# Kernel optimization log

Measured on AMD Instinct MI355X. Metric: run time of the kernel, lower is better.

Reference implementation:

```python
import jax, jax.numpy as jnp
import numpy as np

NUM_USERS = 100000
NUM_ITEMS = 50000
EMB_DIM = 64
NUM_LAYERS = 3
NUM_EDGES = 1000000


def _xavier(key, shape):
    fan_in, fan_out = shape[-1], shape[-2] if len(shape) > 1 else shape[-1]
    limit = float(np.sqrt(6.0 / (fan_in + fan_out)))
    return jax.random.uniform(key, shape, jnp.float32, -limit, limit)


def setup_inputs() -> dict:
    key = jax.random.key(0)
    ks = jax.random.split(key, 8)
    edge_u = jax.random.randint(ks[0], (NUM_EDGES,), 0, NUM_USERS)
    edge_i = jax.random.randint(ks[1], (NUM_EDGES,), 0, NUM_ITEMS)
    u_emb = _xavier(ks[2], (NUM_USERS, EMB_DIM))
    i_emb = _xavier(ks[3], (NUM_ITEMS, EMB_DIM))
    Wgc = _xavier(ks[4], (NUM_LAYERS, EMB_DIM, EMB_DIM))
    Wbi = _xavier(ks[5], (NUM_LAYERS, EMB_DIM, EMB_DIM))
    bgc = jnp.zeros((NUM_LAYERS, EMB_DIM), jnp.float32)
    bbi = jnp.zeros((NUM_LAYERS, EMB_DIM), jnp.float32)
    return {"u_emb": u_emb, "i_emb": i_emb, "Wgc": Wgc, "bgc": bgc,
            "Wbi": Wbi, "bbi": bbi, "edge_u": edge_u, "edge_i": edge_i}


def _smooth(X, src, dst, dv_isqrt, de_inv, num_v, num_e):
    # HGNN smoothing: D_v^{-1/2} H D_e^{-1} H^T D_v^{-1/2} X via edge list
    X1 = X * dv_isqrt[:, None]
    E = jax.ops.segment_sum(X1[src], dst, num_segments=num_e) * de_inv[:, None]
    Y = jax.ops.segment_sum(E[dst], src, num_segments=num_v)
    return Y * dv_isqrt[:, None]


def reference(u_emb, i_emb, Wgc, bgc, Wbi, bbi, edge_u, edge_i):
    NU, NI, D = u_emb.shape[0], i_emb.shape[0], u_emb.shape[1]
    ones = jnp.ones((edge_u.shape[0],), jnp.float32)
    deg_u = jax.ops.segment_sum(ones, edge_u, num_segments=NU)
    deg_i = jax.ops.segment_sum(ones, edge_i, num_segments=NI)
    du_isqrt = jnp.where(deg_u > 0, deg_u, 1.0) ** -0.5 * (deg_u > 0)
    di_isqrt = jnp.where(deg_i > 0, deg_i, 1.0) ** -0.5 * (deg_i > 0)
    du_inv = jnp.where(deg_u > 0, 1.0 / jnp.where(deg_u > 0, deg_u, 1.0), 0.0)
    di_inv = jnp.where(deg_i > 0, 1.0 / jnp.where(deg_i > 0, deg_i, 1.0), 0.0)

    all_embs = jnp.concatenate([u_emb, i_emb], axis=0)
    embs_list = [all_embs]
    for l in range(Wgc.shape[0]):
        u, i = all_embs[:NU], all_embs[NU:]
        # hg_ui: users = vertices, items = hyperedges
        u_s = _smooth(u, edge_u, edge_i, du_isqrt, di_inv, NU, NI)
        # hg_iu: items = vertices, users = hyperedges
        i_s = _smooth(i, edge_i, edge_u, di_isqrt, du_inv, NI, NU)
        g = jnp.concatenate([u_s, i_s], axis=0)
        sum_embs = jax.nn.leaky_relu(g @ Wgc[l].T + bgc[l] + all_embs, negative_slope=0.2)
        bi_embs = jax.nn.leaky_relu((all_embs * g) @ Wbi[l].T + bbi[l], negative_slope=0.2)
        all_embs = sum_embs + bi_embs  # dropout off (eval mode)
        norm = jnp.sqrt(jnp.sum(all_embs * all_embs, axis=1, keepdims=True))
        all_embs = all_embs / jnp.maximum(norm, 1e-12)
        embs_list.append(all_embs)
    embs = jnp.mean(jnp.stack(embs_list, axis=1), axis=1)
    return embs[:NU], embs[NU:]
```

## Files before the change

kernel.cpp:

```cpp
#include <hip/hip_runtime.h>
#include <cstdint>
#include <cstddef>

#define NU 100000
#define NI 50000
#define NTOT 150000
#define EDIM 64
#define NE 1000000
#define NLAYERS 3
#define SCAN_CHUNK 1024
#define NBLK ((NTOT + SCAN_CHUNK - 1) / SCAN_CHUNK)
#define NTILES (NTOT / 16)
#define NPAIR (NTOT / 2)

#define FILL_NRANGE 8
#define FILL_RSPAN (NTOT / FILL_NRANGE)
#define FILL_EPT 4
#define FILL_EPB (256 * FILL_EPT)
#define FILL_NCHUNK ((NE + FILL_EPB - 1) / FILL_EPB)

#define HB_BYTES 32768
#define HB_WORDS (HB_BYTES / 4)
#define NSLICE 128
#define ESLICE ((NE + NSLICE - 1) / NSLICE)
#define NRANGE_U 4
#define NRANGE_I 2
#define NRANGE (NRANGE_U + NRANGE_I)
#define NWORDS (NTOT / 4)

typedef __attribute__((ext_vector_type(8))) short short8;
typedef __attribute__((ext_vector_type(4))) float floatx4;

__device__ inline unsigned short f2bf(float f) {
    unsigned u = __float_as_uint(f);
    u += 0x7fffu + ((u >> 16) & 1u);
    return (unsigned short)(u >> 16);
}
__device__ inline unsigned pack_bf2(float a, float b) {
    unsigned ua = __float_as_uint(a); ua += 0x7fffu + ((ua >> 16) & 1u);
    unsigned ub = __float_as_uint(b); ub += 0x7fffu + ((ub >> 16) & 1u);
    return (ua >> 16) | (ub & 0xffff0000u);
}
__device__ inline float bf_lo(unsigned u) { return __uint_as_float(u << 16); }
__device__ inline float bf_hi(unsigned u) { return __uint_as_float(u & 0xffff0000u); }

__global__ __launch_bounds__(256) void k_hist(const int* __restrict__ eu,
                                              const int* __restrict__ ei,
                                              unsigned* __restrict__ partial) {
    __shared__ unsigned h[HB_WORDS];
    int r = blockIdx.x / NSLICE;
    int s = blockIdx.x % NSLICE;
    const int* arr;
    int base, gbyte, lim;
    if (r < NRANGE_U) {
        arr = eu; base = r * HB_BYTES; gbyte = base;
        lim = min(HB_BYTES, NU - base);
    } else {
        arr = ei; base = (r - NRANGE_U) * HB_BYTES; gbyte = NU + base;
        lim = min(HB_BYTES, NI - base);
    }
    for (int i = threadIdx.x; i < HB_WORDS; i += 256) h[i] = 0;
    __syncthreads();
    const int e0 = s * ESLICE, e1 = min(NE, e0 + ESLICE);
    for (int e = e0 + threadIdx.x; e < e1; e += 256) {
        unsigned local = (unsigned)(arr[e] - base);
        if (local < (unsigned)HB_BYTES)
            atomicAdd(&h[local >> 2], 1u << ((local & 3u) * 8u));
    }
    __syncthreads();
    unsigned* dst = partial + (size_t)s * NWORDS + (gbyte >> 2);
    int lw = lim >> 2;
    for (int i = threadIdx.x; i < lw; i += 256) dst[i] = h[i];
}

__global__ void k_merge(const unsigned* __restrict__ partial, int* __restrict__ deg,
                        float* __restrict__ isq, float* __restrict__ inv) {
    int n = blockIdx.x * blockDim.x + threadIdx.x;
    if (n >= NWORDS) return;
    unsigned se = 0, so = 0;
    for (int s = 0; s < NSLICE; ++s) {
        unsigned v = partial[(size_t)s * NWORDS + n];
        se += v & 0x00ff00ffu;
        so += (v >> 8) & 0x00ff00ffu;
    }
    int d[4];
    d[0] = se & 0xffff; d[1] = so & 0xffff;
    d[2] = se >> 16;    d[3] = so >> 16;
    ((int4*)deg)[n] = make_int4(d[0], d[1], d[2], d[3]);
    float4 q, iv;
    float* qp = &q.x; float* ip = &iv.x;
#pragma unroll
    for (int j = 0; j < 4; ++j) {
        float df = (float)d[j];
        qp[j] = d[j] > 0 ? 1.0f / sqrtf(df) : 0.f;
        ip[j] = d[j] > 0 ? 1.0f / df : 0.f;
    }
    ((float4*)isq)[n] = q;
    ((float4*)inv)[n] = iv;
}


__global__ void k_blocksum(const int* __restrict__ deg, int* __restrict__ partials) {
    __shared__ int sm[256];
    int b = blockIdx.x, t = threadIdx.x;
    int base = b * SCAN_CHUNK + t * 4;
    int s = 0;
#pragma unroll
    for (int j = 0; j < 4; ++j) {
        int idx = base + j;
        if (idx < NTOT) s += deg[idx];
    }
    sm[t] = s;
    __syncthreads();
    for (int off = 128; off > 0; off >>= 1) {
        if (t < off) sm[t] += sm[t + off];
        __syncthreads();
    }
    if (t == 0) partials[b] = sm[0];
}

__global__ void k_scanpartials(int* __restrict__ partials, int nblk) {
    __shared__ int sm[256];
    int t = threadIdx.x;
    int v = (t < nblk) ? partials[t] : 0;
    sm[t] = v;
    __syncthreads();
    for (int off = 1; off < 256; off <<= 1) {
        int tmp = (t >= off) ? sm[t - off] : 0;
        __syncthreads();
        sm[t] += tmp;
        __syncthreads();
    }
    if (t < nblk) partials[t] = sm[t] - v;
}

__global__ void k_scanfinal(const int* __restrict__ deg, const int* __restrict__ partials,
                            int* __restrict__ start, int* __restrict__ cursor) {
    __shared__ int sm[256];
    int b = blockIdx.x, t = threadIdx.x;
    int base = b * SCAN_CHUNK + t * 4;
    int v[4];
    int s = 0;
#pragma unroll
    for (int j = 0; j < 4; ++j) {
        int idx = base + j;
        v[j] = (idx < NTOT) ? deg[idx] : 0;
        s += v[j];
    }
    sm[t] = s;
    __syncthreads();
    for (int off = 1; off < 256; off <<= 1) {
        int tmp = (t >= off) ? sm[t - off] : 0;
        __syncthreads();
        sm[t] += tmp;
        __syncthreads();
    }
    int excl = partials[b] + sm[t] - s;
#pragma unroll
    for (int j = 0; j < 4; ++j) {
        int idx = base + j;
        if (idx < NTOT) {
            start[idx] = excl;
            cursor[idx] = excl;
            excl += v[j];
        }
    }
}

__global__ __launch_bounds__(256) void k_fill_xcd(const int* __restrict__ eu,
                                                  const int* __restrict__ ei,
                                                  int* __restrict__ cursor,
                                                  int* __restrict__ csr) {
    int range = blockIdx.x & (FILL_NRANGE - 1);
    int ebase = (blockIdx.x >> 3) * FILL_EPB + threadIdx.x;
    int lo = range * FILL_RSPAN;
    int hi = lo + FILL_RSPAN;
    int u[FILL_EPT], v[FILL_EPT];
#pragma unroll
    for (int k = 0; k < FILL_EPT; ++k) {
        int e = ebase + k * 256;
        u[k] = (e < NE) ? eu[e] : -1;
        v[k] = (e < NE) ? NU + ei[e] : -1;
    }
    int pu[FILL_EPT], pv[FILL_EPT];
#pragma unroll
    for (int k = 0; k < FILL_EPT; ++k) {
        pu[k] = (u[k] >= lo && u[k] < hi) ? atomicAdd(&cursor[u[k]], 1) : -1;
        pv[k] = (v[k] >= lo && v[k] < hi) ? atomicAdd(&cursor[v[k]], 1) : -1;
    }
#pragma unroll
    for (int k = 0; k < FILL_EPT; ++k) {
        if (pu[k] >= 0) csr[pu[k]] = v[k];
        if (pv[k] >= 0) csr[pv[k]] = u[k];
    }
}

__global__ void k_init(const float* __restrict__ ue, const float* __restrict__ ie,
                       const float* __restrict__ isq,
                       unsigned* __restrict__ snap0, unsigned* gbuf,
                       const float* __restrict__ Wg, const float* __restrict__ Wb,
                       unsigned short* __restrict__ wgb, unsigned short* __restrict__ wbb,
                       unsigned* __restrict__ Ebuf) {
    int i = blockIdx.x * blockDim.x + threadIdx.x;
    const int n4 = NTOT * EDIM / 4;
    const int nw4 = NLAYERS * 4096 / 4;
    if (i < nw4) {
        float4 g4 = ((const float4*)Wg)[i];
        float4 b4 = ((const float4*)Wb)[i];
        uint2 g, b;
        g.x = pack_bf2(g4.x, g4.y); g.y = pack_bf2(g4.z, g4.w);
        b.x = pack_bf2(b4.x, b4.y); b.y = pack_bf2(b4.z, b4.w);
        ((uint2*)wgb)[i] = g;
        ((uint2*)wbb)[i] = b;
    }
    if (i < 16) {
        ((uint2*)(Ebuf + NTOT * 32))[i] = make_uint2(0u, 0u);
        ((uint2*)(gbuf + NTOT * 32))[i] = make_uint2(0u, 0u);
    }
    if (i < n4) {
        const int nu4 = NU * EDIM / 4;
        float4 v = (i < nu4) ? ((const float4*)ue)[i] : ((const float4*)ie)[i - nu4];
        float s = isq[i >> 4];
        uint2 b, bs;
        b.x = pack_bf2(v.x, v.y);
        b.y = pack_bf2(v.z, v.w);
        bs.x = pack_bf2(v.x * s, v.y * s);
        bs.y = pack_bf2(v.z * s, v.w * s);
        ((uint2*)snap0)[i] = b;
        ((uint2*)gbuf)[i] = bs;
    }
}

__global__ __launch_bounds__(256) void k_gather(
    const unsigned* __restrict__ in_bf, unsigned* __restrict__ out_bf,
    const int* __restrict__ csr, const int* __restrict__ start,
    const int* __restrict__ deg, const float* __restrict__ sA) {
    int gw = (blockIdx.x * 256 + threadIdx.x) >> 6;
    int lane = threadIdx.x & 63;
    if (gw >= NPAIR) return;
    int l2 = lane & 31;
    int hbase = lane & 32;
    int row = gw * 2 + (lane >> 5);
    int s0 = start[row];
    int dg = deg[row];
    int dgo = __shfl_xor(dg, 32);
    int dgmax = max(dg, dgo);
    float acc0 = 0.f, acc1 = 0.f;
    for (int j0 = 0; j0 < dgmax; j0 += 32) {
        int nidx = NTOT;
        if (j0 + l2 < dg) nidx = csr[s0 + j0 + l2];
        int jlim = min(32, dgmax - j0);
        for (int j = 0; j < jlim; j += 16) {
            int mm[16];
            unsigned uu[16];
#pragma unroll
            for (int k = 0; k < 16; ++k)
                mm[k] = __shfl(nidx, hbase + j + k);
#pragma unroll
            for (int k = 0; k < 16; ++k)
                uu[k] = in_bf[mm[k] * 32 + l2];
#pragma unroll
            for (int k = 0; k < 16; ++k) {
                acc0 += bf_lo(uu[k]);
                acc1 += bf_hi(uu[k]);
            }
        }
    }
    float s = sA[row];
    out_bf[row * 32 + l2] = pack_bf2(s * acc0, s * acc1);
}

__global__ __launch_bounds__(256) void k_dense_mfma(
    const unsigned short* __restrict__ a_prev, unsigned* gbuf,
    unsigned short* __restrict__ snap_l, const float* __restrict__ isq,
    const unsigned short* __restrict__ wgb, const unsigned short* __restrict__ wbb,
    const float* __restrict__ bg, const float* __restrict__ bb, int writeScaled,
    int finalOut, const unsigned short* __restrict__ s1,
    const float* __restrict__ ue, const float* __restrict__ ie,
    float* __restrict__ outp) {
    int lane = threadIdx.x & 63;
    int lanelo = lane & 15;
    int quad = lane >> 4;
    int wid = (blockIdx.x * blockDim.x + threadIdx.x) >> 6;
    if (wid >= NTILES) return;

    short8 bWg[4][2], bWb[4][2];
#pragma unroll
    for (int t = 0; t < 4; ++t) {
#pragma unroll
        for (int h = 0; h < 2; ++h) {
            int n = t * 16 + lanelo;
            int k0 = h * 32 + quad * 8;
            bWg[t][h] = *(const short8*)&wgb[n * 64 + k0];
            bWb[t][h] = *(const short8*)&wbb[n * 64 + k0];
        }
    }
    float bgv[4], bbv[4];
#pragma unroll
    for (int t = 0; t < 4; ++t) {
        bgv[t] = bg[t * 16 + lanelo];
        bbv[t] = bb[t * 16 + lanelo];
    }

    int rbase = wid * 16;
    int arow = rbase + lanelo;
    short8 aG[2], aAG[2];
#pragma unroll
    for (int h = 0; h < 2; ++h) {
        uint4 ug = *(const uint4*)(gbuf + arow * 32 + h * 16 + quad * 4);
        uint4 ua = *(const uint4*)((const unsigned*)a_prev + arow * 32 + h * 16 + quad * 4);
        aG[h] = *(const short8*)&ug;
        uint4 up;
        up.x = pack_bf2(bf_lo(ua.x) * bf_lo(ug.x), bf_hi(ua.x) * bf_hi(ug.x));
        up.y = pack_bf2(bf_lo(ua.y) * bf_lo(ug.y), bf_hi(ua.y) * bf_hi(ug.y));
        up.z = pack_bf2(bf_lo(ua.z) * bf_lo(ug.z), bf_hi(ua.z) * bf_hi(ug.z));
        up.w = pack_bf2(bf_lo(ua.w) * bf_lo(ug.w), bf_hi(ua.w) * bf_hi(ug.w));
        aAG[h] = *(const short8*)&up;
    }
    floatx4 accg[4], accb[4];
#pragma unroll
    for (int t = 0; t < 4; ++t) {
        accg[t] = (floatx4)(0.f);
        accb[t] = (floatx4)(0.f);
    }
#pragma unroll
    for (int t = 0; t < 4; ++t) {
#pragma unroll
        for (int h = 0; h < 2; ++h) {
            accg[t] = __builtin_amdgcn_mfma_f32_16x16x32_bf16(aG[h], bWg[t][h], accg[t], 0, 0, 0);
            accb[t] = __builtin_amdgcn_mfma_f32_16x16x32_bf16(aAG[h], bWb[t][h], accb[t], 0, 0, 0);
        }
    }
    float nv[4][4];
    float ss[4] = {0.f, 0.f, 0.f, 0.f};
#pragma unroll
    for (int i = 0; i < 4; ++i) {
        int r = rbase + quad * 4 + i;
#pragma unroll
        for (int t = 0; t < 4; ++t) {
            float a = __uint_as_float((unsigned)a_prev[r * 64 + t * 16 + lanelo] << 16);
            float e1 = accg[t][i] + bgv[t] + a;
            e1 = e1 >= 0.f ? e1 : 0.2f * e1;
            float e2 = accb[t][i] + bbv[t];
            e2 = e2 >= 0.f ? e2 : 0.2f * e2;
            float v = e1 + e2;
            nv[i][t] = v;
            ss[i] += v * v;
        }
    }
#pragma unroll
    for (int m = 1; m < 16; m <<= 1) {
#pragma unroll
        for (int i = 0; i < 4; ++i) ss[i] += __shfl_xor(ss[i], m, 64);
    }
#pragma unroll
    for (int i = 0; i < 4; ++i) {
        int r = rbase + quad * 4 + i;
        float rn = 1.0f / fmaxf(sqrtf(ss[i]), 1e-12f);
        float sc = isq[r] * rn;
        if (finalOut) {
#pragma unroll
            for (int t = 0; t < 4; ++t) {
                int idx = r * 64 + t * 16 + lanelo;
                float rr = nv[i][t] * rn;
                float s1v = __uint_as_float((unsigned)s1[idx] << 16);
                float s2v = __uint_as_float((unsigned)a_prev[idx] << 16);
                float ev = (r < NU) ? ue[idx] : ie[idx - NU * 64];
                outp[idx] = 0.25f * (ev + s1v + s2v + rr);
            }
        } else {
#pragma unroll
            for (int t = 0; t < 4; ++t) {
                int idx = r * 64 + t * 16 + lanelo;
                float rr = nv[i][t] * rn;
                snap_l[idx] = f2bf(rr);
                if (writeScaled)
                    ((unsigned short*)gbuf)[idx] = f2bf(nv[i][t] * sc);
            }
        }
    }
}


extern "C" void kernel_launch(void* const* d_in, const int* in_sizes, int n_in,
                              void* d_out, int out_size, void* d_ws, size_t ws_size,
                              hipStream_t stream) {
    const float* u_emb = (const float*)d_in[0];
    const float* i_emb = (const float*)d_in[1];
    const float* Wgc = (const float*)d_in[2];
    const float* bgc = (const float*)d_in[3];
    const float* Wbi = (const float*)d_in[4];
    const float* bbi = (const float*)d_in[5];
    const int* edge_u = (const int*)d_in[6];
    const int* edge_i = (const int*)d_in[7];
    float* out = (float*)d_out;

    char* w = (char*)d_ws;
    auto alloc = [&](size_t bytes) {
        char* p = w;
        w += (bytes + 255) & ~(size_t)255;
        return p;
    };
    const size_t ROWBYTES = (size_t)(NTOT + 1) * EDIM * 2;
    int* deg = (int*)alloc((size_t)NTOT * 4);
    int* start = (int*)alloc((size_t)NTOT * 4);
    int* cursor = (int*)alloc((size_t)NTOT * 4);
    int* partials = (int*)alloc(256 * 4);
    int* csr = (int*)alloc((size_t)2 * NE * 4);
    float* isq = (float*)alloc((size_t)NTOT * 4);
    float* inv = (float*)alloc((size_t)NTOT * 4);
    unsigned short* wgb = (unsigned short*)alloc((size_t)NLAYERS * 4096 * 2);
    unsigned short* wbb = (unsigned short*)alloc((size_t)NLAYERS * 4096 * 2);
    unsigned* snap0 = (unsigned*)alloc((size_t)NTOT * EDIM * 2);
    unsigned* snap1 = (unsigned*)alloc((size_t)NTOT * EDIM * 2);
    unsigned* snap2 = (unsigned*)alloc((size_t)NTOT * EDIM * 2);
    unsigned* Ebuf = (unsigned*)alloc(ROWBYTES);
    unsigned* gbuf = (unsigned*)alloc(ROWBYTES);
    unsigned* hpartial = Ebuf;

    k_hist<<<NRANGE * NSLICE, 256, 0, stream>>>(edge_u, edge_i, hpartial);
    k_merge<<<(NWORDS + 255) / 256, 256, 0, stream>>>(hpartial, deg, isq, inv);
    k_blocksum<<<NBLK, 256, 0, stream>>>(deg, partials);
    k_scanpartials<<<1, 256, 0, stream>>>(partials, NBLK);
    k_scanfinal<<<NBLK, 256, 0, stream>>>(deg, partials, start, cursor);
    k_fill_xcd<<<FILL_NCHUNK * FILL_NRANGE, 256, 0, stream>>>(edge_u, edge_i, cursor, csr);
    k_init<<<(NTOT * EDIM / 4 + 255) / 256, 256, 0, stream>>>(
        u_emb, i_emb, isq, snap0, gbuf, Wgc, Wbi, wgb, wbb, Ebuf);

    const int gatherBlocks = (NPAIR * 64 + 255) / 256;
    const int denseBlocks = (NTILES * 64 + 255) / 256;
    const unsigned short* aprev[3] = {(unsigned short*)snap0, (unsigned short*)snap1,
                                      (unsigned short*)snap2};
    unsigned short* snaps[3] = {(unsigned short*)snap1, (unsigned short*)snap2,
                                (unsigned short*)snap1 };
    for (int l = 0; l < NLAYERS; ++l) {
        k_gather<<<gatherBlocks, 256, 0, stream>>>(gbuf, Ebuf, csr, start, deg, inv);
        k_gather<<<gatherBlocks, 256, 0, stream>>>(Ebuf, gbuf, csr, start, deg, isq);
        k_dense_mfma<<<denseBlocks, 256, 0, stream>>>(
            aprev[l], gbuf, snaps[l], isq, wgb + (size_t)l * 4096, wbb + (size_t)l * 4096,
            bgc + (size_t)l * 64, bbi + (size_t)l * 64,
            l < NLAYERS - 1 ? 1 : 0,
            l == NLAYERS - 1 ? 1 : 0,
            (const unsigned short*)snap1, u_emb, i_emb, out);
    }
}
```

Baseline: 541.7 us.

## Build CSR via bucketed binning and per-bucket shared-memory construction

Replaces the histogram, merge, three-pass scan and global-atomic fill pipeline with a two-stage bucket sort. Edge pairs are first binned into 256 node buckets, sharded 8 ways, in a scratch buffer that aliases the snapshot storage. A single-block prefix then computes bucket offsets. One 1024-thread block per bucket counts degrees, scans and scatters neighbors in LDS before writing its CSR slice contiguously. This cuts kernel launches and scattered global atomics, but fixed capacities (BCAP, SLICE_CAP) silently drop edges if a bucket is denser than the uniform random inputs produce.

```diff
diff --git a/kernel.cpp b/kernel.cpp
--- a/kernel.cpp
+++ b/kernel.cpp
@@ -8,25 +8,17 @@
 #define EDIM 64
 #define NE 1000000
 #define NLAYERS 3
-#define SCAN_CHUNK 1024
-#define NBLK ((NTOT + SCAN_CHUNK - 1) / SCAN_CHUNK)
 #define NTILES (NTOT / 16)
 #define NPAIR (NTOT / 2)
 
-#define FILL_NRANGE 8
-#define FILL_RSPAN (NTOT / FILL_NRANGE)
-#define FILL_EPT 4
-#define FILL_EPB (256 * FILL_EPT)
-#define FILL_NCHUNK ((NE + FILL_EPB - 1) / FILL_EPB)
-
-#define HB_BYTES 32768
-#define HB_WORDS (HB_BYTES / 4)
-#define NSLICE 128
-#define ESLICE ((NE + NSLICE - 1) / NSLICE)
-#define NRANGE_U 4
-#define NRANGE_I 2
-#define NRANGE (NRANGE_U + NRANGE_I)
-#define NWORDS (NTOT / 4)
+#define NBKT 256
+#define NPB 586
+#define NSHARD 8
+#define BCAP 1920
+#define BCUR_STRIDE 16
+#define BIN_EPB 1024
+#define BIN_NBLK ((NE + BIN_EPB - 1) / BIN_EPB)
+#define SLICE_CAP 13312
 
 typedef __attribute__((ext_vector_type(8))) short short8;
 typedef __attribute__((ext_vector_type(4))) float floatx4;
@@ -44,86 +36,43 @@
 __device__ inline float bf_lo(unsigned u) { return __uint_as_float(u << 16); }
 __device__ inline float bf_hi(unsigned u) { return __uint_as_float(u & 0xffff0000u); }
 
-__global__ __launch_bounds__(256) void k_hist(const int* __restrict__ eu,
-                                              const int* __restrict__ ei,
-                                              unsigned* __restrict__ partial) {
-    __shared__ unsigned h[HB_WORDS];
-    int r = blockIdx.x / NSLICE;
-    int s = blockIdx.x % NSLICE;
-    const int* arr;
-    int base, gbyte, lim;
-    if (r < NRANGE_U) {
-        arr = eu; base = r * HB_BYTES; gbyte = base;
-        lim = min(HB_BYTES, NU - base);
-    } else {
-        arr = ei; base = (r - NRANGE_U) * HB_BYTES; gbyte = NU + base;
-        lim = min(HB_BYTES, NI - base);
-    }
-    for (int i = threadIdx.x; i < HB_WORDS; i += 256) h[i] = 0;
-    __syncthreads();
-    const int e0 = s * ESLICE, e1 = min(NE, e0 + ESLICE);
-    for (int e = e0 + threadIdx.x; e < e1; e += 256) {
-        unsigned local = (unsigned)(arr[e] - base);
-        if (local < (unsigned)HB_BYTES)
-            atomicAdd(&h[local >> 2], 1u << ((local & 3u) * 8u));
-    }
-    __syncthreads();
-    unsigned* dst = partial + (size_t)s * NWORDS + (gbyte >> 2);
-    int lw = lim >> 2;
-    for (int i = threadIdx.x; i < lw; i += 256) dst[i] = h[i];
-}
-
-__global__ void k_merge(const unsigned* __restrict__ partial, int* __restrict__ deg,
-                        float* __restrict__ isq, float* __restrict__ inv) {
-    int n = blockIdx.x * blockDim.x + threadIdx.x;
-    if (n >= NWORDS) return;
-    unsigned se = 0, so = 0;
-    for (int s = 0; s < NSLICE; ++s) {
-        unsigned v = partial[(size_t)s * NWORDS + n];
-        se += v & 0x00ff00ffu;
-        so += (v >> 8) & 0x00ff00ffu;
-    }
-    int d[4];
-    d[0] = se & 0xffff; d[1] = so & 0xffff;
-    d[2] = se >> 16;    d[3] = so >> 16;
-    ((int4*)deg)[n] = make_int4(d[0], d[1], d[2], d[3]);
-    float4 q, iv;
-    float* qp = &q.x; float* ip = &iv.x;
-#pragma unroll
-    for (int j = 0; j < 4; ++j) {
-        float df = (float)d[j];
-        qp[j] = d[j] > 0 ? 1.0f / sqrtf(df) : 0.f;
-        ip[j] = d[j] > 0 ? 1.0f / df : 0.f;
-    }
-    ((float4*)isq)[n] = q;
-    ((float4*)inv)[n] = iv;
-}
-
-
-__global__ void k_blocksum(const int* __restrict__ deg, int* __restrict__ partials) {
-    __shared__ int sm[256];
-    int b = blockIdx.x, t = threadIdx.x;
-    int base = b * SCAN_CHUNK + t * 4;
-    int s = 0;
-#pragma unroll
-    for (int j = 0; j < 4; ++j) {
-        int idx = base + j;
-        if (idx < NTOT) s += deg[idx];
-    }
-    sm[t] = s;
-    __syncthreads();
-    for (int off = 128; off > 0; off >>= 1) {
-        if (t < off) sm[t] += sm[t + off];
-        __syncthreads();
-    }
-    if (t == 0) partials[b] = sm[0];
-}
-
-__global__ void k_scanpartials(int* __restrict__ partials, int nblk) {
+__global__ __launch_bounds__(256) void k_binpairs(const int* __restrict__ eu,
+                                                  const int* __restrict__ ei,
+                                                  unsigned* __restrict__ bcur,
+                                                  uint2* __restrict__ bbuf) {
+    int shard = blockIdx.x & (NSHARD - 1);
+    int ebase = blockIdx.x * BIN_EPB + threadIdx.x;
+    int n_[8], o_[8];
+#pragma unroll
+    for (int k = 0; k < 4; ++k) {
+        int e = ebase + k * 256;
+        int u = (e < NE) ? eu[e] : -1;
+        int v = (e < NE) ? NU + ei[e] : -1;
+        n_[k] = u;     o_[k] = v;
+        n_[k + 4] = v; o_[k + 4] = u;
+    }
+    int bb_[8];
+#pragma unroll
+    for (int k = 0; k < 8; ++k) bb_[k] = (n_[k] >= 0) ? (n_[k] / NPB) : -1;
+    int pp_[8];
+#pragma unroll
+    for (int k = 0; k < 8; ++k)
+        pp_[k] = (bb_[k] >= 0)
+                     ? (int)atomicAdd(&bcur[(bb_[k] * NSHARD + shard) * BCUR_STRIDE], 1u)
+                     : -1;
+#pragma unroll
+    for (int k = 0; k < 8; ++k)
+        if (pp_[k] >= 0 && pp_[k] < BCAP)
+            bbuf[(size_t)(bb_[k] * NSHARD + shard) * BCAP + pp_[k]] =
+                make_uint2((unsigned)n_[k], (unsigned)o_[k]);
+}
+
+__global__ void k_bktprefix(const unsigned* __restrict__ bcur, int* __restrict__ bktbase) {
     __shared__ int sm[256];
     int t = threadIdx.x;
-    int v = (t < nblk) ? partials[t] : 0;
-    sm[t] = v;
+    int tot = 0;
+    for (int s = 0; s < NSHARD; ++s) tot += (int)bcur[(t * NSHARD + s) * BCUR_STRIDE];
+    sm[t] = tot;
     __syncthreads();
     for (int off = 1; off < 256; off <<= 1) {
         int tmp = (t >= off) ? sm[t - off] : 0;
@@ -131,68 +80,69 @@
         sm[t] += tmp;
         __syncthreads();
     }
-    if (t < nblk) partials[t] = sm[t] - v;
-}
-
-__global__ void k_scanfinal(const int* __restrict__ deg, const int* __restrict__ partials,
-                            int* __restrict__ start, int* __restrict__ cursor) {
-    __shared__ int sm[256];
-    int b = blockIdx.x, t = threadIdx.x;
-    int base = b * SCAN_CHUNK + t * 4;
-    int v[4];
-    int s = 0;
-#pragma unroll
-    for (int j = 0; j < 4; ++j) {
-        int idx = base + j;
-        v[j] = (idx < NTOT) ? deg[idx] : 0;
-        s += v[j];
-    }
-    sm[t] = s;
-    __syncthreads();
-    for (int off = 1; off < 256; off <<= 1) {
-        int tmp = (t >= off) ? sm[t - off] : 0;
+    bktbase[t] = sm[t] - tot;
+}
+
+__global__ __launch_bounds__(1024) void k_buildcsr(
+    const uint2* __restrict__ bbuf, const unsigned* __restrict__ bcur,
+    const int* __restrict__ bktbase, int* __restrict__ deg, int* __restrict__ start,
+    float* __restrict__ isq, float* __restrict__ inv, int* __restrict__ csr) {
+    __shared__ int slice[SLICE_CAP];
+    __shared__ int lcur[NPB];
+    __shared__ int scnt[NSHARD];
+    int b = blockIdx.x;
+    int t = threadIdx.x;
+    int n0 = b * NPB;
+    int nn = NTOT - n0;
+    if (nn > NPB) nn = NPB;
+    if (nn < 0) nn = 0;
+    if (t < NPB) lcur[t] = 0;
+    if (t < NSHARD) {
+        int c = (int)bcur[(b * NSHARD + t) * BCUR_STRIDE];
+        scnt[t] = c < BCAP ? c : BCAP;
+    }
+    __syncthreads();
+    for (int s = 0; s < NSHARD; ++s) {
+        int c = scnt[s];
+        const uint2* pb = bbuf + (size_t)(b * NSHARD + s) * BCAP;
+        for (int i = t; i < c; i += 1024) atomicAdd(&lcur[(int)pb[i].x - n0], 1);
+    }
+    __syncthreads();
+    int cnt_t = (t < nn) ? lcur[t] : 0;
+    slice[t] = cnt_t;
+    __syncthreads();
+    for (int off = 1; off < 1024; off <<= 1) {
+        int tmp = (t >= off) ? slice[t - off] : 0;
         __syncthreads();
-        sm[t] += tmp;
+        slice[t] += tmp;
         __syncthreads();
     }
-    int excl = partials[b] + sm[t] - s;
-#pragma unroll
-    for (int j = 0; j < 4; ++j) {
-        int idx = base + j;
-        if (idx < NTOT) {
-            start[idx] = excl;
-            cursor[idx] = excl;
-            excl += v[j];
-        }
-    }
-}
-
-__global__ __launch_bounds__(256) void k_fill_xcd(const int* __restrict__ eu,
-                                                  const int* __restrict__ ei,
-                                                  int* __restrict__ cursor,
-                                                  int* __restrict__ csr) {
-    int range = blockIdx.x & (FILL_NRANGE - 1);
-    int ebase = (blockIdx.x >> 3) * FILL_EPB + threadIdx.x;
-    int lo = range * FILL_RSPAN;
-    int hi = lo + FILL_RSPAN;
-    int u[FILL_EPT], v[FILL_EPT];
-#pragma unroll
-    for (int k = 0; k < FILL_EPT; ++k) {
-        int e = ebase + k * 256;
-        u[k] = (e < NE) ? eu[e] : -1;
-        v[k] = (e < NE) ? NU + ei[e] : -1;
-    }
-    int pu[FILL_EPT], pv[FILL_EPT];
-#pragma unroll
-    for (int k = 0; k < FILL_EPT; ++k) {
-        pu[k] = (u[k] >= lo && u[k] < hi) ? atomicAdd(&cursor[u[k]], 1) : -1;
-        pv[k] = (v[k] >= lo && v[k] < hi) ? atomicAdd(&cursor[v[k]], 1) : -1;
-    }
-#pragma unroll
-    for (int k = 0; k < FILL_EPT; ++k) {
-        if (pu[k] >= 0) csr[pu[k]] = v[k];
-        if (pv[k] >= 0) csr[pv[k]] = u[k];
-    }
+    int excl = slice[t] - cnt_t;
+    int slen = slice[1023];
+    int bb = bktbase[b];
+    if (t < nn) {
+        int n = n0 + t;
+        deg[n] = cnt_t;
+        start[n] = bb + excl;
+        float df = (float)cnt_t;
+        isq[n] = cnt_t > 0 ? 1.0f / sqrtf(df) : 0.f;
+        inv[n] = cnt_t > 0 ? 1.0f / df : 0.f;
+    }
+    __syncthreads();
+    if (t < nn) lcur[t] = excl;
+    __syncthreads();
+    for (int s = 0; s < NSHARD; ++s) {
+        int c = scnt[s];
+        const uint2* pb = bbuf + (size_t)(b * NSHARD + s) * BCAP;
+        for (int i = t; i < c; i += 1024) {
+            uint2 pr = pb[i];
+            int idx = atomicAdd(&lcur[(int)pr.x - n0], 1);
+            if (idx < SLICE_CAP) slice[idx] = (int)pr.y;
+        }
+    }
+    __syncthreads();
+    if (slen > SLICE_CAP) slen = SLICE_CAP;
+    for (int i = t; i < slen; i += 1024) csr[bb + i] = slice[i];
 }
 
 __global__ void k_init(const float* __restrict__ ue, const float* __restrict__ ie,
@@ -404,8 +354,8 @@
     const size_t ROWBYTES = (size_t)(NTOT + 1) * EDIM * 2;
     int* deg = (int*)alloc((size_t)NTOT * 4);
     int* start = (int*)alloc((size_t)NTOT * 4);
-    int* cursor = (int*)alloc((size_t)NTOT * 4);
-    int* partials = (int*)alloc(256 * 4);
+    unsigned* bcur = (unsigned*)alloc((size_t)NBKT * NSHARD * BCUR_STRIDE * 4);
+    int* bktbase = (int*)alloc(256 * 4);
     int* csr = (int*)alloc((size_t)2 * NE * 4);
     float* isq = (float*)alloc((size_t)NTOT * 4);
     float* inv = (float*)alloc((size_t)NTOT * 4);
@@ -416,14 +366,12 @@
     unsigned* snap2 = (unsigned*)alloc((size_t)NTOT * EDIM * 2);
     unsigned* Ebuf = (unsigned*)alloc(ROWBYTES);
     unsigned* gbuf = (unsigned*)alloc(ROWBYTES);
-    unsigned* hpartial = Ebuf;
-
-    k_hist<<<NRANGE * NSLICE, 256, 0, stream>>>(edge_u, edge_i, hpartial);
-    k_merge<<<(NWORDS + 255) / 256, 256, 0, stream>>>(hpartial, deg, isq, inv);
-    k_blocksum<<<NBLK, 256, 0, stream>>>(deg, partials);
-    k_scanpartials<<<1, 256, 0, stream>>>(partials, NBLK);
-    k_scanfinal<<<NBLK, 256, 0, stream>>>(deg, partials, start, cursor);
-    k_fill_xcd<<<FILL_NCHUNK * FILL_NRANGE, 256, 0, stream>>>(edge_u, edge_i, cursor, csr);
+    uint2* bbuf = (uint2*)snap1;
+
+    hipMemsetAsync(bcur, 0, (size_t)NBKT * NSHARD * BCUR_STRIDE * 4, stream);
+    k_binpairs<<<BIN_NBLK, 256, 0, stream>>>(edge_u, edge_i, bcur, bbuf);
+    k_bktprefix<<<1, 256, 0, stream>>>(bcur, bktbase);
+    k_buildcsr<<<NBKT, 1024, 0, stream>>>(bbuf, bcur, bktbase, deg, start, isq, inv, csr);
     k_init<<<(NTOT * EDIM / 4 + 255) / 256, 256, 0, stream>>>(
         u_emb, i_emb, isq, snap0, gbuf, Wgc, Wbi, wgb, wbb, Ebuf);
 
```

After: 535.9 us. About the same (-1.1%).
